# Kernel tuning notes

Hardware: AMD Instinct MI355X
Metric: run time of the kernel (lower is better)

## Reference

```python
import jax, jax.numpy as jnp
import numpy as np
from jax import lax


def setup_inputs() -> dict:
    key = jax.random.key(0)
    ks = jax.random.split(key, 12)
    B, T = 64, 256
    H, EN, ET, D = 512, 256, 256, 256  # hidden, embN, embT, embT_dyn (==ET since embedding_sizeT_dyn=None)
    VN, VT, VS = 300, 1000, 100       # vocab_sizeN, vocab_sizeT, num static ids (static_x_ids = range(100))
    s = 0.05
    ar = jnp.arange(VT)
    inp = {}
    inp["n_input"] = jax.random.randint(ks[0], (B, T), 0, VN)
    inp["t_input"] = jax.random.randint(ks[1], (B, T), 0, VT)
    inp["is_static_vocab"] = ar < VS                      # membership test (t in static_x_ids)
    inp["static2dense"] = jnp.where(ar < VS, ar, 0)       # static id -> row in embeddingT
    inp["dynamic2dense"] = jnp.where(ar >= VS, ar - VS, 0)  # dynamic id -> dense dynamic slot
    inp["embN"] = jax.random.normal(ks[2], (VN, EN)) * s
    inp["embT"] = jax.random.normal(ks[3], (VS, ET)) * s
    inp["W_ih"] = jax.random.normal(ks[4], (4 * H, EN + ET)) * s
    inp["W_hh"] = jax.random.normal(ks[5], (4 * H, H)) * s
    inp["b_ih"] = jax.random.normal(ks[6], (4 * H,)) * s
    inp["b_hh"] = jax.random.normal(ks[7], (4 * H,)) * s
    inp["Wd_ih"] = jax.random.normal(ks[8], (4 * D, EN + H)) * s
    inp["Wd_hh"] = jax.random.normal(ks[9], (4 * D, D)) * s
    inp["bd_ih"] = jax.random.normal(ks[10], (4 * D,)) * s
    inp["bd_hh"] = jax.random.normal(ks[11], (4 * D,)) * s
    inp["hid_init"] = jnp.zeros((H,))
    inp["cell_init"] = jnp.zeros((H,))
    inp["dyn_init_h"] = jnp.zeros((1, D))  # anonym_type='pure_zeros'
    inp["dyn_init_c"] = jnp.zeros((1, D))
    return inp


def _lstm_cell(x, h, c, Wi, Wh, bi, bh):
    # torch.nn.LSTMCell gate order: i, f, g, o
    g = x @ Wi.T + bi + h @ Wh.T + bh
    i, f, gg, o = jnp.split(g, 4, axis=-1)
    c2 = jax.nn.sigmoid(f) * c + jax.nn.sigmoid(i) * jnp.tanh(gg)
    return jax.nn.sigmoid(o) * jnp.tanh(c2), c2


def reference(n_input, t_input, is_static_vocab, static2dense, dynamic2dense,
              embN, embT, W_ih, W_hh, b_ih, b_hh,
              Wd_ih, Wd_hh, bd_ih, bd_hh,
              hid_init, cell_init, dyn_init_h, dyn_init_c):
    # The torch module's growing (lookup_table, de_h, de_c) cache is equivalent to
    # per-(batch, dynamic-token) state arrays Hd/Cd [B, V_dyn, D] with a 'seen' flag:
    # each (b, token) pair owns exactly one cache slot that is read/updated in place.
    B, T = n_input.shape
    H = hid_init.shape[0]
    D = dyn_init_h.shape[-1]
    VD = int(dynamic2dense.max()) + 1  # number of dynamic vocab slots (static at setup)
    bidx = jnp.arange(B)
    init_h = jnp.broadcast_to(dyn_init_h, (B, D))
    init_c = jnp.broadcast_to(dyn_init_c, (B, D))

    def step(carry, xt):
        h, c, seen, Hd, Cd = carry
        nt, tt = xt
        is_st = is_static_vocab[tt]            # [B] bool
        didx = dynamic2dense[tt]               # [B] dynamic slot (garbage 0 for static rows, masked below)
        sn = seen[bidx, didx]                  # was this (b, token) created before?
        hd_prev = jnp.where(sn[:, None], Hd[bidx, didx], init_h)
        cd_prev = jnp.where(sn[:, None], Cd[bidx, didx], init_c)
        n_emb = embN[nt]                       # [B, EN] (dropout=0 -> plain lookup)
        # emb_transform is identity (embedding_sizeT_dyn is None)
        h_tensor = jnp.where(is_st[:, None], embT[static2dense[tt]], hd_prev)  # [B, ET]
        h_new, c_new = _lstm_cell(jnp.concatenate([n_emb, h_tensor], 1), h, c, W_ih, W_hh, b_ih, b_hh)
        # dynamic-embedding LSTM: input is (n_emb, previous main hidden h)
        hd_new, cd_new = _lstm_cell(jnp.concatenate([n_emb, h], 1), hd_prev, cd_prev, Wd_ih, Wd_hh, bd_ih, bd_hh)
        dyn = (~is_st)[:, None]
        Hd = Hd.at[bidx, didx].set(jnp.where(dyn, hd_new, Hd[bidx, didx]))
        Cd = Cd.at[bidx, didx].set(jnp.where(dyn, cd_new, Cd[bidx, didx]))
        seen = seen.at[bidx, didx].set(sn | (~is_st))
        return (h_new, c_new, seen, Hd, Cd), h_new

    h0 = jnp.broadcast_to(hid_init, (B, H)) + 0.0
    c0 = jnp.broadcast_to(cell_init, (B, H)) + 0.0
    carry0 = (h0, c0,
              jnp.zeros((B, VD), dtype=bool),
              jnp.zeros((B, VD, D), dtype=embN.dtype),
              jnp.zeros((B, VD, D), dtype=embN.dtype))
    _, outs = lax.scan(step, carry0, (n_input.T, t_input.T))  # outs: [T, B, H]
    return jnp.transpose(outs, (1, 0, 2))                     # [B, T, H]
```

## Files before the change

### kernel.cpp

```cpp
#include <hip/hip_runtime.h>


typedef _Float16 f16;
typedef _Float16 f16x8 __attribute__((ext_vector_type(8)));
typedef float f32x4 __attribute__((ext_vector_type(4)));

#define B_ 64
#define T_ 256
#define H_ 512
#define EN_ 256
#define ET_ 256
#define D_ 256
#define VN_ 300
#define VS_ 100

#define NB_MAIN_ 128
#define NB_DYN_ 64
#define NBLK_ 192
#define NTHR_ 256
#define NSH_ 64
#define PER_SHARD_ (NBLK_ / NSH_)
#define POLL_CAP_ (1u << 22)

static constexpr size_t OFF_CNT  = 0;
static constexpr size_t OFF_EMBN = 4096;
static constexpr size_t OFF_EMBT = OFF_EMBN + (size_t)VN_ * EN_ * 2;
static constexpr size_t OFF_DINH = OFF_EMBT + (size_t)VS_ * ET_ * 2;
static constexpr size_t OFF_PREV = OFF_DINH + 1024;
static constexpr size_t OFF_HH   = OFF_PREV + (size_t)T_ * B_ * 4;
static constexpr size_t OFF_HD   = OFF_HH + (size_t)(T_ + 1) * B_ * H_ * 2;
static constexpr size_t OFF_CD   = OFF_HD + (size_t)T_ * B_ * D_ * 2;
static constexpr size_t WS_NEED  = OFF_CD + (size_t)T_ * B_ * D_ * 4;

struct RnnParams {
  const int* n_input; const int* t_input; const int* s2d;
  const float* W_ih; const float* W_hh; const float* b_ih; const float* b_hh;
  const float* Wd_ih; const float* Wd_hh; const float* bd_ih; const float* bd_hh;
  const float* cell_init; const float* dyn_init_c;
  const f16* embN16; const f16* embT16; const f16* dynih16;
  const int* prev;
  f16* Hhist; f16* HdHist; float* CdHist;
  float* out; unsigned* cnt;
};

__device__ __forceinline__ float sigm(float x) { return 1.f / (1.f + __expf(-x)); }
__device__ __forceinline__ float tanh_fast(float x) {
  float e = __expf(2.f * x);
  return 1.f - 2.f / (e + 1.f);
}

__device__ __forceinline__ void cstore8(void* p, unsigned long long v) {
  __hip_atomic_store((unsigned long long*)p, v, __ATOMIC_RELAXED,
                     __HIP_MEMORY_SCOPE_AGENT);
}
__device__ __forceinline__ void cstore16(void* p, f32x4 v) {
  asm volatile("global_store_dwordx4 %0, %1, off sc0 sc1"
               :: "v"(p), "v"(v) : "memory");
}

__global__ void setup_kernel(const float* embN, const float* embT,
                             const float* hid_init, const float* dyn_init_h,
                             f16* embN16, f16* embT16, f16* dynih16,
                             f16* Hhist0, unsigned* cnt) {
  int i = blockIdx.x * blockDim.x + threadIdx.x;
  if (i < 1024)      cnt[i] = 0u;
  if (i < VN_ * EN_) embN16[i] = (f16)embN[i];
  if (i < VS_ * ET_) embT16[i] = (f16)embT[i];
  if (i < D_)        dynih16[i] = (f16)dyn_init_h[i];
  if (i < B_ * H_)   Hhist0[i] = (f16)hid_init[i & (H_ - 1)];
  __threadfence();
}

__global__ void prev_kernel(const int* t_input, const int* s2d, int* prev) {
  int idx = blockIdx.x * blockDim.x + threadIdx.x;
  if (idx < B_ * T_) {
    int b = idx / T_, t = idx % T_;
    int tt = t_input[b * T_ + t];
    int p = -1;
    if (s2d[tt] != tt) {
      for (int q = t - 1; q >= 0; --q)
        if (t_input[b * T_ + q] == tt) { p = q; break; }
    }
    prev[t * B_ + b] = p;
  }
  __threadfence();
}

__device__ __forceinline__ void resolve(const RnnParams& p, bool isDyn, int t, int b,
                                        int tprev,
                                        const f16** aN, const f16** aX,
                                        const float** aC, int* dynw, int* rc) {
  const int nt = p.n_input[b * T_ + t];
  aN[b] = p.embN16 + (size_t)nt * EN_;
  const int tt = p.t_input[b * T_ + t];
  const int pv = p.prev[t * B_ + b];
  rc[b] = (pv >= 0 && pv == tprev) ? 1 : 0;
  const f16* hd = (pv >= 0) ? (p.HdHist + ((size_t)pv * B_ + b) * D_) : p.dynih16;
  const int s2 = p.s2d[tt];
  const bool st = (s2 == tt);
  if (!isDyn) {
    aX[b] = st ? (p.embT16 + (size_t)s2 * ET_) : hd;
  } else {
    aX[b] = hd;
    aC[b] = (pv >= 0) ? (p.CdHist + ((size_t)pv * B_ + b) * D_) : p.dyn_init_c;
    dynw[b] = st ? 0 : 1;
  }
}

__global__ __launch_bounds__(NTHR_, 1) void rnn_main(RnnParams p) {
  const int blk  = blockIdx.x;
  const int tid  = threadIdx.x;
  const int wave = tid >> 6;
  const int lane = tid & 63;
  const bool isDyn = (blk >= NB_MAIN_);
  const int u0 = isDyn ? (blk - NB_MAIN_) * 4 : blk * 4;

  __threadfence();

  __shared__ float s_bias[16];
  __shared__ float s_scr[64][17];
  __shared__ const f16*  s_aN[2][64];
  __shared__ const f16*  s_aX[2][64];
  __shared__ const float* s_aC[2][64];
  __shared__ int s_dynw[2][64];
  __shared__ int s_rc[2][64];

  const int nIdx = lane & 15;
  const int ui = nIdx & 3, gate = nIdx >> 2;
  const int ko = (lane >> 4) * 8;
  f16x8 w[32];
  if (!isDyn) {
    const int r = gate * H_ + u0 + ui;
#pragma unroll
    for (int s = 0; s < 32; ++s) {
      const int k = s * 32 + ko;
      const float* src = (k < 512) ? (p.W_ih + (size_t)r * 512 + k)
                                   : (p.W_hh + (size_t)r * 512 + (k - 512));
      f16x8 v;
#pragma unroll
      for (int j = 0; j < 8; ++j) v[j] = (f16)src[j];
      w[s] = v;
    }
  } else {
    const int r = gate * D_ + u0 + ui;
#pragma unroll
    for (int s = 0; s < 32; ++s) {
      const int k = s * 32 + ko;
      const float* src = (k < 768) ? (p.Wd_ih + (size_t)r * 768 + k)
                                   : (p.Wd_hh + (size_t)r * 256 + (k - 768));
      f16x8 v;
#pragma unroll
      for (int j = 0; j < 8; ++j) v[j] = (f16)src[j];
      w[s] = v;
    }
  }
  if (tid < 16) {
    int g2 = tid >> 2, un2 = tid & 3;
    s_bias[tid] = isDyn ? (p.bd_ih[g2 * D_ + u0 + un2] + p.bd_hh[g2 * D_ + u0 + un2])
                        : (p.b_ih[g2 * H_ + u0 + un2] + p.b_hh[g2 * H_ + u0 + un2]);
  }
  float creg[4] = {0.f, 0.f, 0.f, 0.f};
  if (tid < 64 && !isDyn) {
#pragma unroll
    for (int un = 0; un < 4; ++un) creg[un] = p.cell_init[u0 + un];
  }
  if (tid < 64)
    resolve(p, isDyn, 0, tid, -1, s_aN[0], s_aX[0], s_aC[0], s_dynw[0], s_rc[0]);
  __syncthreads();

  const int b = (wave << 4) + (lane & 15);
  f16x8 pf[16];
  float4 cvp = {0.f, 0.f, 0.f, 0.f};
  {
    const f16* pN = s_aN[0][b];
    const f16* pX = s_aX[0][b];
#pragma unroll
    for (int i = 0; i < 8; ++i) pf[i] = *(const f16x8*)(pN + i * 32 + ko);
#pragma unroll
    for (int i = 0; i < 8; ++i) pf[8 + i] = *(const f16x8*)(pX + i * 32 + ko);
    if (isDyn && tid < 64) cvp = *(const float4*)(s_aC[0][tid] + u0);
  }

  for (int t = 0; t < T_; ++t) {
    const int pb = t & 1;

    const f16* pH = p.Hhist + ((size_t)t * B_ + b) * H_;
    f16x8 hh[16];
#pragma unroll
    for (int i = 0; i < 16; ++i) hh[i] = *(const f16x8*)(pH + i * 32 + ko);
    if (s_rc[pb][b]) {
      const f16* pX = s_aX[pb][b];
#pragma unroll
      for (int i = 0; i < 8; ++i) pf[8 + i] = *(const f16x8*)(pX + i * 32 + ko);
    }

    f32x4 ac[4] = {{0,0,0,0},{0,0,0,0},{0,0,0,0},{0,0,0,0}};
    if (!isDyn) {
#pragma unroll
      for (int i = 0; i < 8; ++i)
        ac[i & 3] = __builtin_amdgcn_mfma_f32_16x16x32_f16(pf[i], w[i], ac[i & 3], 0, 0, 0);
#pragma unroll
      for (int i = 0; i < 8; ++i)
        ac[i & 3] = __builtin_amdgcn_mfma_f32_16x16x32_f16(pf[8 + i], w[8 + i], ac[i & 3], 0, 0, 0);
#pragma unroll
      for (int i = 0; i < 16; ++i)
        ac[i & 3] = __builtin_amdgcn_mfma_f32_16x16x32_f16(hh[i], w[16 + i], ac[i & 3], 0, 0, 0);
    } else {
#pragma unroll
      for (int i = 0; i < 8; ++i)
        ac[i & 3] = __builtin_amdgcn_mfma_f32_16x16x32_f16(pf[i], w[i], ac[i & 3], 0, 0, 0);
#pragma unroll
      for (int i = 0; i < 8; ++i)
        ac[i & 3] = __builtin_amdgcn_mfma_f32_16x16x32_f16(pf[8 + i], w[24 + i], ac[i & 3], 0, 0, 0);
#pragma unroll
      for (int i = 0; i < 16; ++i)
        ac[i & 3] = __builtin_amdgcn_mfma_f32_16x16x32_f16(hh[i], w[8 + i], ac[i & 3], 0, 0, 0);
    }
    f32x4 acc = (ac[0] + ac[1]) + (ac[2] + ac[3]);
#pragma unroll
    for (int j = 0; j < 4; ++j)
      s_scr[(wave << 4) + ((lane >> 4) << 2) + j][lane & 15] = acc[j];
    __syncthreads();

    if (tid < 64) {
      const int eb = tid;
      if (isDyn && s_rc[pb][eb])
        cvp = *(const float4*)(s_aC[pb][eb] + u0);
      float g[16];
#pragma unroll
      for (int n = 0; n < 16; ++n) g[n] = s_scr[eb][n] + s_bias[n];
      if (!isDyn) {
        float4 ho;
        union { f16 h[4]; unsigned long long u; } pk;
#pragma unroll
        for (int un = 0; un < 4; ++un) {
          float c = sigm(g[4 + un]) * creg[un] + sigm(g[un]) * tanh_fast(g[8 + un]);
          creg[un] = c;
          float h = sigm(g[12 + un]) * tanh_fast(c);
          (&ho.x)[un] = h;
          pk.h[un] = (f16)h;
        }
        *(float4*)&p.out[((size_t)eb * T_ + t) * H_ + u0] = ho;
        cstore8(&p.Hhist[((size_t)(t + 1) * B_ + eb) * H_ + u0], pk.u);
      } else {
        const float cold[4] = {cvp.x, cvp.y, cvp.z, cvp.w};
        f32x4 co;
        union { f16 h[4]; unsigned long long u; } pk;
#pragma unroll
        for (int un = 0; un < 4; ++un) {
          float c = sigm(g[4 + un]) * cold[un] + sigm(g[un]) * tanh_fast(g[8 + un]);
          float h = sigm(g[12 + un]) * tanh_fast(c);
          pk.h[un] = (f16)h;
          co[un] = c;
        }
        if (s_dynw[pb][eb]) {
          cstore8(&p.HdHist[((size_t)t * B_ + eb) * D_ + u0], pk.u);
          cstore16(&p.CdHist[((size_t)t * B_ + eb) * D_ + u0], co);
        }
      }
    } else if (tid < 128 && t + 1 < T_) {
      resolve(p, isDyn, t + 1, tid - 64, t,
              s_aN[pb ^ 1], s_aX[pb ^ 1], s_aC[pb ^ 1], s_dynw[pb ^ 1], s_rc[pb ^ 1]);
    }

    if (t + 1 < T_) {
      __syncthreads();
      if (tid == 0)
        __hip_atomic_fetch_add(&p.cnt[(blk & (NSH_ - 1)) << 4], 1u,
                               __ATOMIC_RELAXED, __HIP_MEMORY_SCOPE_AGENT);
      {
        const f16* pN2 = s_aN[pb ^ 1][b];
        const f16* pX2 = s_aX[pb ^ 1][b];
#pragma unroll
        for (int i = 0; i < 8; ++i) pf[i] = *(const f16x8*)(pN2 + i * 32 + ko);
#pragma unroll
        for (int i = 0; i < 8; ++i) pf[8 + i] = *(const f16x8*)(pX2 + i * 32 + ko);
        if (isDyn && tid < 64) cvp = *(const float4*)(s_aC[pb ^ 1][tid] + u0);
      }
      if (tid < NSH_) {
        const unsigned tgt = (unsigned)(t + 1) * PER_SHARD_;
        unsigned it = 0;
        while (__hip_atomic_load(&p.cnt[tid << 4], __ATOMIC_RELAXED,
                                 __HIP_MEMORY_SCOPE_AGENT) < tgt &&
               ++it < POLL_CAP_)
          __builtin_amdgcn_s_sleep(1);
      }
      __syncthreads();
    }
  }
}

extern "C" void kernel_launch(void* const* d_in, const int* in_sizes, int n_in,
                              void* d_out, int out_size, void* d_ws, size_t ws_size,
                              hipStream_t stream) {
  (void)in_sizes; (void)n_in; (void)out_size;
  const int* n_input   = (const int*)d_in[0];
  const int* t_input   = (const int*)d_in[1];
  const int* s2d       = (const int*)d_in[3];
  const float* embN    = (const float*)d_in[5];
  const float* embT    = (const float*)d_in[6];
  const float* W_ih    = (const float*)d_in[7];
  const float* W_hh    = (const float*)d_in[8];
  const float* b_ih    = (const float*)d_in[9];
  const float* b_hh    = (const float*)d_in[10];
  const float* Wd_ih   = (const float*)d_in[11];
  const float* Wd_hh   = (const float*)d_in[12];
  const float* bd_ih   = (const float*)d_in[13];
  const float* bd_hh   = (const float*)d_in[14];
  const float* hid_init  = (const float*)d_in[15];
  const float* cell_init = (const float*)d_in[16];
  const float* dyn_init_h = (const float*)d_in[17];
  const float* dyn_init_c = (const float*)d_in[18];

  char* ws = (char*)d_ws;
  unsigned* cnt  = (unsigned*)(ws + OFF_CNT);
  f16* embN16    = (f16*)(ws + OFF_EMBN);
  f16* embT16    = (f16*)(ws + OFF_EMBT);
  f16* dynih16   = (f16*)(ws + OFF_DINH);
  int* prev      = (int*)(ws + OFF_PREV);
  f16* Hhist     = (f16*)(ws + OFF_HH);
  f16* HdHist    = (f16*)(ws + OFF_HD);
  float* CdHist  = (float*)(ws + OFF_CD);
  if (ws_size < WS_NEED) return;

  setup_kernel<<<dim3((VN_ * EN_ + NTHR_ - 1) / NTHR_), dim3(NTHR_), 0, stream>>>(
      embN, embT, hid_init, dyn_init_h, embN16, embT16, dynih16, Hhist, cnt);
  prev_kernel<<<dim3((B_ * T_ + NTHR_ - 1) / NTHR_), dim3(NTHR_), 0, stream>>>(
      t_input, s2d, prev);

  RnnParams prm;
  prm.n_input = n_input; prm.t_input = t_input; prm.s2d = s2d;
  prm.W_ih = W_ih; prm.W_hh = W_hh; prm.b_ih = b_ih; prm.b_hh = b_hh;
  prm.Wd_ih = Wd_ih; prm.Wd_hh = Wd_hh; prm.bd_ih = bd_ih; prm.bd_hh = bd_hh;
  prm.cell_init = cell_init; prm.dyn_init_c = dyn_init_c;
  prm.embN16 = embN16; prm.embT16 = embT16; prm.dynih16 = dynih16;
  prm.prev = prev; prm.Hhist = Hhist; prm.HdHist = HdHist; prm.CdHist = CdHist;
  prm.out = (float*)d_out; prm.cnt = cnt;

  void* args[] = { &prm };
  hipError_t e = hipLaunchCooperativeKernel((const void*)rnn_main,
                                            dim3(NBLK_), dim3(NTHR_), args, 0, stream);
  if (e != hipSuccess) {
    rnn_main<<<dim3(NBLK_), dim3(NTHR_), 0, stream>>>(prm);
  }
}
```

Baseline: 1.397 ms.

## Replace block barriers with per-wave counters and all-lane gate epilogue

Drops the per-step __syncthreads and block-level shard counters. Each wave now signals its own arrival counter, main and dynamic blocks use separate counter regions, and waves poll counters directly. Readers can therefore wait only on the producers they need, and the prefetch of the next step's embedding and dynamic-state rows moves earlier. The gate epilogue is spread across all 64 lanes, one unit per lane, so 16 lanes no longer do four units each. The hidden history is stored in a k-major interleaved layout to make the h loads coalesce. In exchange there is more atomic polling traffic, scalar 2-byte stores with cache bypass, and subtler memory-ordering correctness.

```diff
diff --git a/kernel.cpp b/kernel.cpp
--- a/kernel.cpp
+++ b/kernel.cpp
@@ -18,12 +18,11 @@
 #define NB_DYN_ 64
 #define NBLK_ 192
 #define NTHR_ 256
-#define NSH_ 64
-#define PER_SHARD_ (NBLK_ / NSH_)
 #define POLL_CAP_ (1u << 22)
+#define DNER_W_ 1024
 
 static constexpr size_t OFF_CNT  = 0;
-static constexpr size_t OFF_EMBN = 4096;
+static constexpr size_t OFF_EMBN = 8192;
 static constexpr size_t OFF_EMBT = OFF_EMBN + (size_t)VN_ * EN_ * 2;
 static constexpr size_t OFF_DINH = OFF_EMBT + (size_t)VS_ * ET_ * 2;
 static constexpr size_t OFF_PREV = OFF_DINH + 1024;
@@ -48,14 +47,8 @@
   float e = __expf(2.f * x);
   return 1.f - 2.f / (e + 1.f);
 }
-
-__device__ __forceinline__ void cstore8(void* p, unsigned long long v) {
-  __hip_atomic_store((unsigned long long*)p, v, __ATOMIC_RELAXED,
-                     __HIP_MEMORY_SCOPE_AGENT);
-}
-__device__ __forceinline__ void cstore16(void* p, f32x4 v) {
-  asm volatile("global_store_dwordx4 %0, %1, off sc0 sc1"
-               :: "v"(p), "v"(v) : "memory");
+__device__ __forceinline__ unsigned cld(const unsigned* w) {
+  return __hip_atomic_load(w, __ATOMIC_RELAXED, __HIP_MEMORY_SCOPE_AGENT);
 }
 
 __global__ void setup_kernel(const float* embN, const float* embT,
@@ -63,11 +56,14 @@
                              f16* embN16, f16* embT16, f16* dynih16,
                              f16* Hhist0, unsigned* cnt) {
   int i = blockIdx.x * blockDim.x + threadIdx.x;
-  if (i < 1024)      cnt[i] = 0u;
+  if (i < 2048)      cnt[i] = 0u;
   if (i < VN_ * EN_) embN16[i] = (f16)embN[i];
   if (i < VS_ * ET_) embT16[i] = (f16)embT[i];
   if (i < D_)        dynih16[i] = (f16)dyn_init_h[i];
-  if (i < B_ * H_)   Hhist0[i] = (f16)hid_init[i & (H_ - 1)];
+  if (i < B_ * H_) {
+    int b = i >> 9, k = i & 511;
+    Hhist0[(k >> 3) * 512 + b * 8 + (k & 7)] = (f16)hid_init[k];
+  }
   __threadfence();
 }
 
@@ -86,24 +82,27 @@
   __threadfence();
 }
 
-__device__ __forceinline__ void resolve(const RnnParams& p, bool isDyn, int t, int b,
-                                        int tprev,
-                                        const f16** aN, const f16** aX,
-                                        const float** aC, int* dynw, int* rc) {
-  const int nt = p.n_input[b * T_ + t];
-  aN[b] = p.embN16 + (size_t)nt * EN_;
-  const int tt = p.t_input[b * T_ + t];
-  const int pv = p.prev[t * B_ + b];
-  rc[b] = (pv >= 0 && pv == tprev) ? 1 : 0;
-  const f16* hd = (pv >= 0) ? (p.HdHist + ((size_t)pv * B_ + b) * D_) : p.dynih16;
+__device__ __forceinline__ void resolve_lane(const RnnParams& p, bool isDyn, int s,
+                                             int bg, int eui, int u0,
+                                             const f16*& pN, const f16*& pX,
+                                             const float*& pC, int& dynw, int& rc) {
+  const int nt = p.n_input[bg * T_ + s];
+  pN = p.embN16 + (size_t)nt * EN_;
+  const int tt = p.t_input[bg * T_ + s];
+  const int pv = p.prev[s * B_ + bg];
+  rc = (pv >= 0 && pv + 2 >= s) ? 1 : 0;
+  const f16* hd = (pv >= 0) ? (p.HdHist + ((size_t)pv * B_ + bg) * D_) : p.dynih16;
   const int s2 = p.s2d[tt];
   const bool st = (s2 == tt);
   if (!isDyn) {
-    aX[b] = st ? (p.embT16 + (size_t)s2 * ET_) : hd;
+    pX = st ? (p.embT16 + (size_t)s2 * ET_) : hd;
+    if (st) rc = 0;
+    dynw = 0;
   } else {
-    aX[b] = hd;
-    aC[b] = (pv >= 0) ? (p.CdHist + ((size_t)pv * B_ + b) * D_) : p.dyn_init_c;
-    dynw[b] = st ? 0 : 1;
+    pX = hd;
+    pC = ((pv >= 0) ? (p.CdHist + ((size_t)pv * B_ + bg) * D_) : p.dyn_init_c)
+         + u0 + eui;
+    dynw = st ? 0 : 1;
   }
 }
 
@@ -117,20 +116,14 @@
 
   __threadfence();
 
-  __shared__ float s_bias[16];
-  __shared__ float s_scr[64][17];
-  __shared__ const f16*  s_aN[2][64];
-  __shared__ const f16*  s_aX[2][64];
-  __shared__ const float* s_aC[2][64];
-  __shared__ int s_dynw[2][64];
-  __shared__ int s_rc[2][64];
+  __shared__ float s_scr[2][4][16][17];
 
   const int nIdx = lane & 15;
-  const int ui = nIdx & 3, gate = nIdx >> 2;
+  const int wui = nIdx & 3, wgate = nIdx >> 2;
   const int ko = (lane >> 4) * 8;
   f16x8 w[32];
   if (!isDyn) {
-    const int r = gate * H_ + u0 + ui;
+    const int r = wgate * H_ + u0 + wui;
 #pragma unroll
     for (int s = 0; s < 32; ++s) {
       const int k = s * 32 + ko;
@@ -142,7 +135,7 @@
       w[s] = v;
     }
   } else {
-    const int r = gate * D_ + u0 + ui;
+    const int r = wgate * D_ + u0 + wui;
 #pragma unroll
     for (int s = 0; s < 32; ++s) {
       const int k = s * 32 + ko;
@@ -154,44 +147,65 @@
       w[s] = v;
     }
   }
-  if (tid < 16) {
-    int g2 = tid >> 2, un2 = tid & 3;
-    s_bias[tid] = isDyn ? (p.bd_ih[g2 * D_ + u0 + un2] + p.bd_hh[g2 * D_ + u0 + un2])
-                        : (p.b_ih[g2 * H_ + u0 + un2] + p.b_hh[g2 * H_ + u0 + un2]);
-  }
-  float creg[4] = {0.f, 0.f, 0.f, 0.f};
-  if (tid < 64 && !isDyn) {
-#pragma unroll
-    for (int un = 0; un < 4; ++un) creg[un] = p.cell_init[u0 + un];
-  }
-  if (tid < 64)
-    resolve(p, isDyn, 0, tid, -1, s_aN[0], s_aX[0], s_aC[0], s_dynw[0], s_rc[0]);
-  __syncthreads();
-
-  const int b = (wave << 4) + (lane & 15);
+
+  const int bq  = lane & 15;
+  const int eui = lane >> 4;
+  const int bg  = (wave << 4) + bq;
+  const int hoff = (eui << 9) + (bq << 3) + (wave << 7);
+  const unsigned arriveW = isDyn
+      ? (unsigned)(DNER_W_ + ((((blk - NB_MAIN_) << 2) | wave) & 31) * 16)
+      : (unsigned)(((((blk << 2) | wave)) & 63) * 16);
+
+  float bias_g[4];
+#pragma unroll
+  for (int g = 0; g < 4; ++g)
+    bias_g[g] = isDyn ? (p.bd_ih[g * D_ + u0 + eui] + p.bd_hh[g * D_ + u0 + eui])
+                      : (p.b_ih[g * H_ + u0 + eui] + p.b_hh[g * H_ + u0 + eui]);
+  float creg = isDyn ? 0.f : p.cell_init[u0 + eui];
+
+  const f16 *pN, *pX; const float* pC = p.dyn_init_c; int dynw = 0, rc = 0;
+  resolve_lane(p, isDyn, 0, bg, eui, u0, pN, pX, pC, dynw, rc);
   f16x8 pf[16];
-  float4 cvp = {0.f, 0.f, 0.f, 0.f};
-  {
-    const f16* pN = s_aN[0][b];
-    const f16* pX = s_aX[0][b];
-#pragma unroll
-    for (int i = 0; i < 8; ++i) pf[i] = *(const f16x8*)(pN + i * 32 + ko);
-#pragma unroll
-    for (int i = 0; i < 8; ++i) pf[8 + i] = *(const f16x8*)(pX + i * 32 + ko);
-    if (isDyn && tid < 64) cvp = *(const float4*)(s_aC[0][tid] + u0);
-  }
+#pragma unroll
+  for (int i = 0; i < 8; ++i) pf[i] = *(const f16x8*)(pN + i * 32 + ko);
+#pragma unroll
+  for (int i = 0; i < 8; ++i) pf[8 + i] = *(const f16x8*)(pX + i * 32 + ko);
+  float cvp = isDyn ? *pC : 0.f;
 
   for (int t = 0; t < T_; ++t) {
     const int pb = t & 1;
 
-    const f16* pH = p.Hhist + ((size_t)t * B_ + b) * H_;
+    if (t) {
+      const unsigned* wp = p.cnt + (lane << 4);
+      const unsigned tgt = 8u * (unsigned)t;
+      unsigned it = 0;
+      while (__any(cld(wp) < tgt) && ++it < POLL_CAP_)
+        __builtin_amdgcn_s_sleep(1);
+      __builtin_amdgcn_sched_barrier(0);
+    }
+
+    const f16* pH2 = p.Hhist + (size_t)t * 32768 + hoff;
     f16x8 hh[16];
 #pragma unroll
-    for (int i = 0; i < 16; ++i) hh[i] = *(const f16x8*)(pH + i * 32 + ko);
-    if (s_rc[pb][b]) {
-      const f16* pX = s_aX[pb][b];
-#pragma unroll
-      for (int i = 0; i < 8; ++i) pf[8 + i] = *(const f16x8*)(pX + i * 32 + ko);
+    for (int i = 0; i < 16; ++i) hh[i] = *(const f16x8*)(pH2 + i * 2048);
+
+    if (__any(rc)) {
+      const unsigned* wp = p.cnt + DNER_W_ + ((lane & 31) << 4);
+      const unsigned tgt = 8u * (unsigned)t;
+      unsigned it = 0;
+      while (__any(cld(wp) < tgt) && ++it < POLL_CAP_)
+        __builtin_amdgcn_s_sleep(1);
+      if (rc) {
+#pragma unroll
+        for (int i = 0; i < 8; ++i)
+          asm volatile("global_load_dwordx4 %0, %1, off sc0 sc1"
+                       : "=&v"(pf[8 + i]) : "v"(pX + i * 32 + ko));
+        if (isDyn)
+          asm volatile("global_load_dword %0, %1, off sc0 sc1"
+                       : "=&v"(cvp) : "v"(pC));
+      }
+      asm volatile("s_waitcnt vmcnt(0)" ::: "memory");
+      __builtin_amdgcn_sched_barrier(0);
     }
 
     f32x4 ac[4] = {{0,0,0,0},{0,0,0,0},{0,0,0,0},{0,0,0,0}};
@@ -217,75 +231,61 @@
         ac[i & 3] = __builtin_amdgcn_mfma_f32_16x16x32_f16(hh[i], w[8 + i], ac[i & 3], 0, 0, 0);
     }
     f32x4 acc = (ac[0] + ac[1]) + (ac[2] + ac[3]);
+
 #pragma unroll
     for (int j = 0; j < 4; ++j)
-      s_scr[(wave << 4) + ((lane >> 4) << 2) + j][lane & 15] = acc[j];
-    __syncthreads();
-
-    if (tid < 64) {
-      const int eb = tid;
-      if (isDyn && s_rc[pb][eb])
-        cvp = *(const float4*)(s_aC[pb][eb] + u0);
-      float g[16];
-#pragma unroll
-      for (int n = 0; n < 16; ++n) g[n] = s_scr[eb][n] + s_bias[n];
-      if (!isDyn) {
-        float4 ho;
-        union { f16 h[4]; unsigned long long u; } pk;
-#pragma unroll
-        for (int un = 0; un < 4; ++un) {
-          float c = sigm(g[4 + un]) * creg[un] + sigm(g[un]) * tanh_fast(g[8 + un]);
-          creg[un] = c;
-          float h = sigm(g[12 + un]) * tanh_fast(c);
-          (&ho.x)[un] = h;
-          pk.h[un] = (f16)h;
-        }
-        *(float4*)&p.out[((size_t)eb * T_ + t) * H_ + u0] = ho;
-        cstore8(&p.Hhist[((size_t)(t + 1) * B_ + eb) * H_ + u0], pk.u);
-      } else {
-        const float cold[4] = {cvp.x, cvp.y, cvp.z, cvp.w};
-        f32x4 co;
-        union { f16 h[4]; unsigned long long u; } pk;
-#pragma unroll
-        for (int un = 0; un < 4; ++un) {
-          float c = sigm(g[4 + un]) * cold[un] + sigm(g[un]) * tanh_fast(g[8 + un]);
-          float h = sigm(g[12 + un]) * tanh_fast(c);
-          pk.h[un] = (f16)h;
-          co[un] = c;
-        }
-        if (s_dynw[pb][eb]) {
-          cstore8(&p.HdHist[((size_t)t * B_ + eb) * D_ + u0], pk.u);
-          cstore16(&p.CdHist[((size_t)t * B_ + eb) * D_ + u0], co);
-        }
+      s_scr[pb][wave][(eui << 2) + j][bq] = acc[j];
+    asm volatile("s_waitcnt lgkmcnt(0)" ::: "memory");
+    __builtin_amdgcn_sched_barrier(0);
+    const float g0 = s_scr[pb][wave][bq][eui]      + bias_g[0];
+    const float g1 = s_scr[pb][wave][bq][4 + eui]  + bias_g[1];
+    const float g2 = s_scr[pb][wave][bq][8 + eui]  + bias_g[2];
+    const float g3 = s_scr[pb][wave][bq][12 + eui] + bias_g[3];
+
+    if (!isDyn) {
+      const float c = sigm(g1) * creg + sigm(g0) * tanh_fast(g2);
+      creg = c;
+      const float h = sigm(g3) * tanh_fast(c);
+      p.out[((size_t)bg * T_ + t) * H_ + u0 + eui] = h;
+      const int u = u0 + eui;
+      f16* hp = p.Hhist + (size_t)(t + 1) * 32768 + ((u >> 3) << 9) + (bg << 3) + (u & 7);
+      union { f16 hf; unsigned short us; } pk; pk.hf = (f16)h;
+      asm volatile("global_store_short %0, %1, off sc0 sc1"
+                   :: "v"(hp), "v"((unsigned)pk.us) : "memory");
+    } else {
+      const float c = sigm(g1) * cvp + sigm(g0) * tanh_fast(g2);
+      const float h = sigm(g3) * tanh_fast(c);
+      if (dynw) {
+        f16* hp = p.HdHist + ((size_t)t * B_ + bg) * D_ + u0 + eui;
+        float* cp = p.CdHist + ((size_t)t * B_ + bg) * D_ + u0 + eui;
+        union { f16 hf; unsigned short us; } pk; pk.hf = (f16)h;
+        asm volatile("global_store_short %0, %1, off sc0 sc1"
+                     :: "v"(hp), "v"((unsigned)pk.us) : "memory");
+        asm volatile("global_store_dword %0, %1, off sc0 sc1"
+                     :: "v"(cp), "v"(c) : "memory");
       }
-    } else if (tid < 128 && t + 1 < T_) {
-      resolve(p, isDyn, t + 1, tid - 64, t,
-              s_aN[pb ^ 1], s_aX[pb ^ 1], s_aC[pb ^ 1], s_dynw[pb ^ 1], s_rc[pb ^ 1]);
     }
 
     if (t + 1 < T_) {
-      __syncthreads();
-      if (tid == 0)
-        __hip_atomic_fetch_add(&p.cnt[(blk & (NSH_ - 1)) << 4], 1u,
-                               __ATOMIC_RELAXED, __HIP_MEMORY_SCOPE_AGENT);
-      {
-        const f16* pN2 = s_aN[pb ^ 1][b];
-        const f16* pX2 = s_aX[pb ^ 1][b];
-#pragma unroll
-        for (int i = 0; i < 8; ++i) pf[i] = *(const f16x8*)(pN2 + i * 32 + ko);
-#pragma unroll
-        for (int i = 0; i < 8; ++i) pf[8 + i] = *(const f16x8*)(pX2 + i * 32 + ko);
-        if (isDyn && tid < 64) cvp = *(const float4*)(s_aC[pb ^ 1][tid] + u0);
-      }
-      if (tid < NSH_) {
-        const unsigned tgt = (unsigned)(t + 1) * PER_SHARD_;
+      asm volatile("s_waitcnt vmcnt(0)" ::: "memory");
+      if (lane == 0)
+        __hip_atomic_fetch_add(&p.cnt[arriveW], 1u, __ATOMIC_RELAXED,
+                               __HIP_MEMORY_SCOPE_AGENT);
+
+      resolve_lane(p, isDyn, t + 1, bg, eui, u0, pN, pX, pC, dynw, rc);
+      if (t >= 2) {
+        const unsigned* wp = p.cnt + DNER_W_ + ((lane & 31) << 4);
+        const unsigned tgt = 8u * (unsigned)(t - 1);
         unsigned it = 0;
-        while (__hip_atomic_load(&p.cnt[tid << 4], __ATOMIC_RELAXED,
-                                 __HIP_MEMORY_SCOPE_AGENT) < tgt &&
-               ++it < POLL_CAP_)
+        while (__any(cld(wp) < tgt) && ++it < POLL_CAP_)
           __builtin_amdgcn_s_sleep(1);
       }
-      __syncthreads();
+      __builtin_amdgcn_sched_barrier(0);
+#pragma unroll
+      for (int i = 0; i < 8; ++i) pf[i] = *(const f16x8*)(pN + i * 32 + ko);
+#pragma unroll
+      for (int i = 0; i < 8; ++i) pf[8 + i] = *(const f16x8*)(pX + i * 32 + ko);
+      if (isDyn) cvp = *pC;
     }
   }
 }
```

Result: slower. 1.994 ms (+42.7%).
